# Optimization experiments

Hardware: AMD Instinct MI355X
Metric: run time of the kernel (lower is better)

## Reference

```python
import jax, jax.numpy as jnp
import numpy as np
from jax import lax

EPS = 1e-20

def _conv(x, w, b):
    # stride-2 conv, padding=1, NCHW/OIHW (torch Conv2d semantics)
    y = lax.conv_general_dilated(x, w, (2, 2), ((1, 1), (1, 1)),
                                 dimension_numbers=('NCHW', 'OIHW', 'NCHW'))
    return y + b[None, :, None, None]

def _deconv(x, w, b):
    # ConvTranspose2d(k=4, s=2, p=1): doubles spatial dims (== SAME transpose padding)
    y = lax.conv_transpose(x, w, (2, 2), 'SAME',
                           dimension_numbers=('NCHW', 'OIHW', 'NCHW'))
    return y + b[None, :, None, None]

def _enc_switch(h, win, bin_, wout, bout, wsw, bsw, gnoise):
    r = jax.nn.relu(h)
    hid = jnp.einsum('bd,kds->bks', r, win) + bin_            # [B,K,S]
    y_logits = jnp.einsum('bks,ks->bk', hid, wsw) + bsw       # [B,K]
    g = -jnp.log(gnoise + EPS)                                # Gumbel noise
    y_soft = jax.nn.softmax(y_logits + g, axis=1)
    y_index = jnp.argmax(y_soft, axis=1)                      # [B]
    one_hot = jax.nn.one_hot(y_index, y_logits.shape[1], dtype=y_soft.dtype)
    y_hard = one_hot - lax.stop_gradient(y_soft) + y_soft     # straight-through
    outs = jnp.einsum('bks,ksd->bkd', hid, wout) + bout       # [B,K,192]
    out = jnp.take_along_axis(outs, y_index[:, None, None], axis=1)[:, 0]
    gate = jnp.take_along_axis(y_hard, y_index[:, None], axis=1)  # [B,1] (training gate)
    return h + out * gate, y_logits, y_index, y_hard

def _dec_switch(h, win, bin_, wout, bout, y_index, y_hard):
    r = jax.nn.relu(h)
    hid = jnp.einsum('bd,kds->bks', r, win) + bin_
    outs = jnp.einsum('bks,ksd->bkd', hid, wout) + bout
    out = jnp.take_along_axis(outs, y_index[:, None, None], axis=1)[:, 0]
    gate = jnp.take_along_axis(y_hard, y_index[:, None], axis=1)
    return h + out * gate

def setup_inputs() -> dict:
    key = jax.random.key(0)
    B, C, L, D, K, S = 1024, 3, 10, 192, 10, 10
    ks = jax.random.split(key, 48)
    def n(i, shape, s=0.05):
        return jax.random.normal(ks[i], shape, jnp.float32) * s
    return {
        'x': jax.random.uniform(ks[0], (B, C, 64, 64), jnp.float32),
        'gnoise': jax.random.exponential(ks[1], (L, B, K)).astype(jnp.float32),
        'znoise': jax.random.normal(ks[2], (B, L), jnp.float32),
        'cw1': n(3, (32, C, 4, 4)), 'cb1': n(4, (32,)),
        'cw2': n(5, (32, 32, 4, 4)), 'cb2': n(6, (32,)),
        'cw3': n(7, (64, 32, 4, 4)), 'cb3': n(8, (64,)),
        'cw4': n(9, (64, 64, 4, 4)), 'cb4': n(10, (64,)),
        'fc_w': n(11, (1024, D)), 'fc_b': n(12, (D,)),
        'ein_w': n(13, (L, K, D, S)), 'ein_b': n(14, (L, K, S)),
        'eout_w': n(15, (L, K, S, D)), 'eout_b': n(16, (L, K, D)),
        'esw_w': n(17, (L, K, S)), 'esw_b': n(18, (L, K)),
        'mean_w': n(19, (D, L)), 'mean_b': n(20, (L,)),
        'lv_w': n(21, (D, L)), 'lv_b': n(22, (L,)),
        'fcl_w': n(23, (L, D)), 'fcl_b': n(24, (D,)),
        'din_w': n(25, (L, K, D, S)), 'din_b': n(26, (L, K, S)),
        'dout_w': n(27, (L, K, S, D)), 'dout_b': n(28, (L, K, D)),
        'dfc_w': n(29, (D, 1024)), 'dfc_b': n(30, (1024,)),
        'dw1': n(31, (64, 64, 4, 4)), 'db1': n(32, (64,)),
        'dw2': n(33, (32, 64, 4, 4)), 'db2': n(34, (32,)),
        'dw3': n(35, (32, 32, 4, 4)), 'db3': n(36, (32,)),
        'dw4': n(37, (C, 32, 4, 4)), 'db4': n(38, (C,)),
    }

def reference(x, gnoise, znoise, cw1, cb1, cw2, cb2, cw3, cb3, cw4, cb4,
              fc_w, fc_b, ein_w, ein_b, eout_w, eout_b, esw_w, esw_b,
              mean_w, mean_b, lv_w, lv_b, fcl_w, fcl_b,
              din_w, din_b, dout_w, dout_b, dfc_w, dfc_b,
              dw1, db1, dw2, db2, dw3, db3, dw4, db4):
    # ---- encoder convs ----
    h = jax.nn.relu(_conv(x, cw1, cb1))
    h = jax.nn.relu(_conv(h, cw2, cb2))
    h = jax.nn.relu(_conv(h, cw3, cb3))
    h = jax.nn.relu(_conv(h, cw4, cb4))           # [B,64,4,4]
    h = h.reshape(-1, 1024) @ fc_w + fc_b         # [B,192]
    # ---- encoder FC switches (sequential over latents) ----
    L = ein_w.shape[0]
    ys_index, ys_hard = [], []
    for i in range(L):
        h, _, yi, yh = _enc_switch(h, ein_w[i], ein_b[i], eout_w[i], eout_b[i],
                                   esw_w[i], esw_b[i], gnoise[i])
        ys_index.append(yi); ys_hard.append(yh)
    r = jax.nn.relu(h)
    z_mean = r @ mean_w + mean_b
    z_logvar = r @ lv_w + lv_b
    # ---- reparameterize ----
    z = znoise * jnp.exp(z_logvar / 2) + z_mean
    # ---- decoder ----
    d = z @ fcl_w + fcl_b
    for i in range(L):
        d = _dec_switch(d, din_w[i], din_b[i], dout_w[i], dout_b[i],
                        ys_index[i], ys_hard[i])
    d = jax.nn.relu(d)
    d = jax.nn.relu(d @ dfc_w + dfc_b)
    d = d.reshape(-1, 64, 4, 4)
    d = jax.nn.relu(_deconv(d, dw1, db1))
    d = jax.nn.relu(_deconv(d, dw2, db2))
    d = jax.nn.relu(_deconv(d, dw3, db3))
    recon_x = _deconv(d, dw4, db4)                # [B,C,64,64] logits
    return recon_x, z, z_mean, z_logvar
```

## Files before the change

kernel.cpp:

```cpp
#include <hip/hip_runtime.h>
#include <hip/hip_bf16.h>
#include <math.h>


#define BATCH 1024

using short8 = __attribute__((ext_vector_type(8))) short;
using f32x4  = __attribute__((ext_vector_type(4))) float;

__device__ __forceinline__ ushort f2bf(float f) {
    uint u = __float_as_uint(f);
    uint r = (u + 0x7fffu + ((u >> 16) & 1u)) >> 16;
    return (ushort)r;
}
__device__ __forceinline__ float bf2f(ushort u) {
    return __uint_as_float(((uint)u) << 16);
}
constexpr int ilog2(int v) { return v <= 1 ? 0 : 1 + ilog2(v >> 1); }

__device__ __forceinline__ void conv_frag_elem(const float* __restrict__ w,
                                               ushort* __restrict__ frag,
                                               int idx, int CIN, int COUT) {
    int NCH = CIN / 32, NT = COUT / 16;
    int j = idx & 7; int lane = (idx >> 3) & 63; int rest = idx >> 9;
    int ntile = rest % NT; rest /= NT;
    int ch = rest % NCH; int tap = rest / NCH;
    int o = ntile * 16 + (lane & 15);
    int i = ch * 32 + (lane >> 4) * 8 + j;
    frag[idx] = f2bf(w[((size_t)(o * CIN + i)) * 16 + tap]);
}
__device__ __forceinline__ void deconv_frag_elem(const float* __restrict__ w,
                                                 ushort* __restrict__ frag,
                                                 int idx, int CIN, int COUT) {
    int NCH = CIN / 32, NT = COUT / 16;
    int j = idx & 7; int lane = (idx >> 3) & 63; int rest = idx >> 9;
    int ntile = rest % NT; rest /= NT;
    int ch = rest % NCH; rest /= NCH;
    int tapidx = rest % 4; int cls = rest / 4;
    int py = cls >> 1, px = cls & 1, a = tapidx >> 1, b = tapidx & 1;
    int tap = (py + 2 * a) * 4 + (px + 2 * b);
    int o = ntile * 16 + (lane & 15);
    int i = ch * 32 + (lane >> 4) * 8 + j;
    frag[idx] = f2bf(w[((size_t)(o * CIN + i)) * 16 + tap]);
}

__global__ __launch_bounds__(256)
void prep_all(const float* __restrict__ cw1, const float* __restrict__ cw2,
              const float* __restrict__ cw3, const float* __restrict__ cw4,
              const float* __restrict__ dw1, const float* __restrict__ dw2,
              const float* __restrict__ dw3, const float* __restrict__ dw4,
              const float* __restrict__ ein_w, const float* __restrict__ fc_w,
              const float* __restrict__ dfc_w,
              ushort* __restrict__ c1g, ushort* __restrict__ c2g,
              ushort* __restrict__ c3g, ushort* __restrict__ c4g,
              ushort* __restrict__ d1g, ushort* __restrict__ d2g,
              ushort* __restrict__ d3g, ushort* __restrict__ d4g,
              ushort* __restrict__ encwTb, ushort* __restrict__ fc1g,
              ushort* __restrict__ dfcg) {
    const int b = blockIdx.x, t = threadIdx.x;
    if (b < 8) {
        int idx = b * 256 + t;
        if (idx < 2048) {
            int j = idx & 7; int lane = (idx >> 3) & 63;
            int ntile = (idx >> 9) & 1; int s = idx >> 10;
            int o = ntile * 16 + (lane & 15);
            int kg = lane >> 4;
            int tap = s * 8 + kg * 2 + (j >> 2);
            int c = j & 3;
            c1g[idx] = (c < 3) ? f2bf(cw1[((size_t)(o * 3 + c)) * 16 + tap]) : (ushort)0;
        }
    } else if (b < 72) {
        conv_frag_elem(cw2, c2g, (b - 8) * 256 + t, 32, 32);
    } else if (b < 200) {
        conv_frag_elem(cw3, c3g, (b - 72) * 256 + t, 32, 64);
    } else if (b < 456) {
        conv_frag_elem(cw4, c4g, (b - 200) * 256 + t, 64, 64);
    } else if (b < 712) {
        deconv_frag_elem(dw1, d1g, (b - 456) * 256 + t, 64, 64);
    } else if (b < 840) {
        deconv_frag_elem(dw2, d2g, (b - 712) * 256 + t, 64, 32);
    } else if (b < 904) {
        deconv_frag_elem(dw3, d3g, (b - 840) * 256 + t, 32, 32);
    } else if (b < 936) {
        int idx = (b - 904) * 256 + t;
        if (idx < 8192) {
            int j = idx & 7; int lane = (idx >> 3) & 63; int rest = idx >> 9;
            int tapidx = rest & 3; int cls = rest >> 2;
            int py = cls >> 1, px = cls & 1, a = tapidx >> 1, bb = tapidx & 1;
            int tap = (py + 2 * a) * 4 + (px + 2 * bb);
            int o = lane & 15;
            int i = (lane >> 4) * 8 + j;
            d4g[idx] = (o < 3) ? f2bf(dw4[((size_t)(o * 32 + i)) * 16 + tap]) : (ushort)0;
        }
    } else if (b < 1686) {
        int idx = (b - 936) * 256 + t;
        if (idx < 192000) {
            int ks = idx % 100;
            int d = (idx / 100) % 192;
            int l = idx / 19200;
            int k = ks / 10, s = ks % 10;
            encwTb[idx] = f2bf(ein_w[(size_t)l * 19200 + k * 1920 + d * 10 + s]);
        }
    } else if (b < 2454) {
        int idx = (b - 1686) * 256 + t;
        int jj = idx & 7; int lane = (idx >> 3) & 63; int rest = idx >> 9;
        int nt = rest % 12, s = rest / 12;
        int k_nat = s * 32 + (lane >> 4) * 8 + jj;
        int d = (k_nat & 63) * 16 + (k_nat >> 6);
        int j = nt * 16 + (lane & 15);
        fc1g[idx] = f2bf(fc_w[(size_t)d * 192 + j]);
    } else {
        int idx = (b - 2454) * 256 + t;
        int jj = idx & 7; int lane = (idx >> 3) & 63; int rest = idx >> 9;
        int nt = rest % 64, s = rest / 64;
        int k = s * 32 + (lane >> 4) * 8 + jj;
        int j_nat = nt * 16 + (lane & 15);
        int d = (j_nat & 63) * 16 + (j_nat >> 6);
        dfcg[idx] = f2bf(dfc_w[(size_t)k * 1024 + d]);
    }
}

__global__ __launch_bounds__(256)
void conv12_fused(const float* __restrict__ x, const ushort* __restrict__ w1frag,
                  const float* __restrict__ b1, const ushort* __restrict__ w2frag,
                  const float* __restrict__ b2, ushort* __restrict__ out) {
    __shared__ ushort mid[576 * 40];
    const int t = threadIdx.x;
    const int lane = t & 63, w = t >> 6;
    const int m = lane & 15, kg = lane >> 4;
    const int h = blockIdx.x & 1, n = blockIdx.x >> 1;
    const int base = 16 * h - 1;
    const float* xb = x + (size_t)n * 12288;

    short8 bf1[4];
    #pragma unroll
    for (int f = 0; f < 4; ++f)
        bf1[f] = *(const short8*)(w1frag + (f << 9) + lane * 8);

    for (int mt = w; mt < 36; mt += 4) {
        const int lp = mt * 16 + m;
        const int lx = lp & 31, lyy = lp >> 5;
        const int my = base + lyy;
        const int iy0 = 2 * my - 1, ix0 = 2 * lx - 1;
        short8 av[2];
        #pragma unroll
        for (int s = 0; s < 2; ++s) {
            short8 a;
            #pragma unroll
            for (int tt = 0; tt < 2; ++tt) {
                const int tap = s * 8 + kg * 2 + tt;
                const int ky = tap >> 2, kx = tap & 3;
                const int iy = iy0 + ky, ix = ix0 + kx;
                float v0 = 0.f, v1 = 0.f, v2 = 0.f;
                if ((unsigned)iy < 64u && (unsigned)ix < 64u) {
                    const float* xr = xb + ((iy << 6) + ix);
                    v0 = xr[0]; v1 = xr[4096]; v2 = xr[8192];
                }
                a[4 * tt + 0] = (short)f2bf(v0);
                a[4 * tt + 1] = (short)f2bf(v1);
                a[4 * tt + 2] = (short)f2bf(v2);
                a[4 * tt + 3] = 0;
            }
            av[s] = a;
        }
        f32x4 acc[2] = {{0,0,0,0},{0,0,0,0}};
        #pragma unroll
        for (int s = 0; s < 2; ++s)
            #pragma unroll
            for (int nt = 0; nt < 2; ++nt)
                acc[nt] = __builtin_amdgcn_mfma_f32_16x16x32_bf16(av[s], bf1[s * 2 + nt], acc[nt], 0, 0, 0);
        #pragma unroll
        for (int nt = 0; nt < 2; ++nt) {
            const int och = (nt << 4) + m;
            const float bv = b1[och];
            #pragma unroll
            for (int r = 0; r < 4; ++r) {
                const int lpr = (mt << 4) + (kg << 2) + r;
                mid[(size_t)lpr * 40 + och] = f2bf(fmaxf(acc[nt][r] + bv, 0.f));
            }
        }
    }
    __syncthreads();
    for (int it = 0; it < 4; ++it) {
        const int u = it * 4 + w;
        const int nt = u & 1, mt2 = u >> 1;
        const int p2 = (mt2 << 4) + m;
        const int ox2 = p2 & 15, ly2 = p2 >> 4;
        const int oy2 = 8 * h + ly2;
        const int iy0 = 2 * oy2 - 1, ix0 = 2 * ox2 - 1;
        f32x4 acc = {0, 0, 0, 0};
        const ushort* wl = w2frag + ((size_t)nt << 9) + lane * 8;
        #pragma unroll
        for (int ky = 0; ky < 4; ++ky) {
            const int iy = iy0 + ky;
            const bool vy = (unsigned)iy < 32u;
            const int liy = iy - base;
            #pragma unroll
            for (int kx = 0; kx < 4; ++kx) {
                const int ix = ix0 + kx;
                const bool v = vy && ((unsigned)ix < 32u);
                short8 a = {0, 0, 0, 0, 0, 0, 0, 0};
                if (v) a = *(const short8*)(mid + (size_t)((liy << 5) + ix) * 40 + kg * 8);
                const short8 b = *(const short8*)(wl + ((size_t)((ky * 4 + kx) * 2) << 9));
                acc = __builtin_amdgcn_mfma_f32_16x16x32_bf16(a, b, acc, 0, 0, 0);
            }
        }
        const int och = (nt << 4) + m;
        const float bv = b2[och];
        ushort* ob = out + ((size_t)n * 256 + 128 * h + (mt2 << 4) + (kg << 2)) * 32;
        #pragma unroll
        for (int r = 0; r < 4; ++r)
            ob[r * 32 + och] = f2bf(fmaxf(acc[r] + bv, 0.f));
    }
}

template<int CIN, int COUT, int HIN, int WIN, int NTW, bool RELU>
__global__ __launch_bounds__(256)
void conv_mfma(const ushort* __restrict__ in, const ushort* __restrict__ wfrag,
               const float* __restrict__ bias, ushort* __restrict__ out) {
    constexpr int HOUT = HIN / 2, WOUT = WIN / 2, NCH = CIN / 32, NT = COUT / 16;
    constexpr int NTG = NT / NTW;
    constexpr int LW = ilog2(WOUT), LH = ilog2(HOUT);
    const int lane = threadIdx.x & 63;
    const int gw = (blockIdx.x << 2) + (threadIdx.x >> 6);
    const int ntg = gw % NTG;
    const int mtile = gw / NTG;
    const int m = lane & 15, kg = lane >> 4;
    const int p = (mtile << 4) + m;
    const int ox = p & (WOUT - 1), oy = (p >> LW) & (HOUT - 1), n = p >> (LW + LH);
    const ushort* ibase = in + (size_t)n * (HIN * WIN * CIN);
    const int iy0 = 2 * oy - 1, ix0 = 2 * ox - 1;
    f32x4 acc[NTW];
    #pragma unroll
    for (int nt = 0; nt < NTW; ++nt) acc[nt] = (f32x4){0, 0, 0, 0};
    const ushort* wl = wfrag + ((size_t)(ntg * NTW) << 9) + lane * 8;
    #pragma unroll
    for (int ky = 0; ky < 4; ++ky) {
        const int iy = iy0 + ky;
        const bool vy = (unsigned)iy < (unsigned)HIN;
        #pragma unroll
        for (int kx = 0; kx < 4; ++kx) {
            const int ix = ix0 + kx;
            const bool v = vy && ((unsigned)ix < (unsigned)WIN);
            const int tap = ky * 4 + kx;
            #pragma unroll
            for (int ch = 0; ch < NCH; ++ch) {
                short8 a = {0, 0, 0, 0, 0, 0, 0, 0};
                if (v) a = *(const short8*)(ibase + (size_t)(iy * WIN + ix) * CIN + ch * 32 + kg * 8);
                #pragma unroll
                for (int nt = 0; nt < NTW; ++nt) {
                    const short8 b = *(const short8*)(wl + ((size_t)((tap * NCH + ch) * NT + nt) << 9));
                    acc[nt] = __builtin_amdgcn_mfma_f32_16x16x32_bf16(a, b, acc[nt], 0, 0, 0);
                }
            }
        }
    }
    ushort* ob = out + (size_t)((mtile << 4) + (kg << 2)) * COUT;
    #pragma unroll
    for (int nt = 0; nt < NTW; ++nt) {
        const int och = ((ntg * NTW + nt) << 4) + m;
        const float bv = bias[och];
        #pragma unroll
        for (int r = 0; r < 4; ++r) {
            float vv = acc[nt][r] + bv;
            if (RELU) vv = fmaxf(vv, 0.f);
            ob[r * COUT + och] = f2bf(vv);
        }
    }
}

template<int CIN, int COUT, int HIN, int WIN, int NTW, bool RELU>
__global__ __launch_bounds__(256)
void deconv_mfma_fused(const ushort* __restrict__ in, const ushort* __restrict__ wfrag,
                       const float* __restrict__ bias, ushort* __restrict__ out) {
    constexpr int HOUT = 2 * HIN, WOUT = 2 * WIN, NCH = CIN / 32, NT = COUT / 16;
    constexpr int NTG = NT / NTW;
    constexpr int LW = ilog2(WIN), LH = ilog2(HIN);
    const int lane = threadIdx.x & 63;
    const int gw = (blockIdx.x << 2) + (threadIdx.x >> 6);
    const int ntg = gw % NTG;
    const int mtile = gw / NTG;
    const int m = lane & 15, kg = lane >> 4;
    const int q = (mtile << 4) + m;
    const int oxh = q & (WIN - 1), oyh = (q >> LW) & (HIN - 1), n = q >> (LW + LH);
    const ushort* ibase = in + (size_t)n * (HIN * WIN * CIN);
    f32x4 acc[4][NTW];
    #pragma unroll
    for (int c = 0; c < 4; ++c)
        #pragma unroll
        for (int nt = 0; nt < NTW; ++nt) acc[c][nt] = (f32x4){0, 0, 0, 0};
    const ushort* wl = wfrag + ((size_t)(ntg * NTW) << 9) + lane * 8;
    #pragma unroll
    for (int ch = 0; ch < NCH; ++ch) {
        short8 nb[3][3];
        #pragma unroll
        for (int dy = 0; dy < 3; ++dy) {
            const int iy = oyh + dy - 1;
            const bool vy = (unsigned)iy < (unsigned)HIN;
            #pragma unroll
            for (int dx = 0; dx < 3; ++dx) {
                const int ix = oxh + dx - 1;
                short8 a = {0, 0, 0, 0, 0, 0, 0, 0};
                if (vy && (unsigned)ix < (unsigned)WIN)
                    a = *(const short8*)(ibase + (size_t)(iy * WIN + ix) * CIN + ch * 32 + kg * 8);
                nb[dy][dx] = a;
            }
        }
        #pragma unroll
        for (int cls = 0; cls < 4; ++cls) {
            const int py = cls >> 1, px = cls & 1;
            #pragma unroll
            for (int ti = 0; ti < 4; ++ti) {
                const int a2 = ti >> 1, b2 = ti & 1;
                #pragma unroll
                for (int nt = 0; nt < NTW; ++nt) {
                    const short8 b = *(const short8*)(wl + ((size_t)(((cls * 4 + ti) * NCH + ch) * NT + nt) << 9));
                    acc[cls][nt] = __builtin_amdgcn_mfma_f32_16x16x32_bf16(nb[py + a2][px + b2], b, acc[cls][nt], 0, 0, 0);
                }
            }
        }
    }
    #pragma unroll
    for (int nt = 0; nt < NTW; ++nt) {
        const int och = ((ntg * NTW + nt) << 4) + m;
        const float bv = bias[och];
        #pragma unroll
        for (int cls = 0; cls < 4; ++cls) {
            const int py = cls >> 1, px = cls & 1;
            #pragma unroll
            for (int r = 0; r < 4; ++r) {
                const int qq = (mtile << 4) + (kg << 2) + r;
                const int oxh2 = qq & (WIN - 1), oyh2 = (qq >> LW) & (HIN - 1), n2 = qq >> (LW + LH);
                const int oy = 2 * oyh2 + py, ox = 2 * oxh2 + px;
                float vv = acc[cls][nt][r] + bv;
                if (RELU) vv = fmaxf(vv, 0.f);
                out[(size_t)((n2 * HOUT + oy) * WOUT + ox) * COUT + och] = f2bf(vv);
            }
        }
    }
}

__global__ __launch_bounds__(256)
void deconv34_fused(const ushort* __restrict__ in, const ushort* __restrict__ w3frag,
                    const float* __restrict__ b3, const ushort* __restrict__ w4frag,
                    const float* __restrict__ b4, float* __restrict__ out) {
    __shared__ ushort mid[20 * 32 * 32];
    const int t = threadIdx.x;
    const int lane = t & 63, w = t >> 6;
    const int m = lane & 15, kg = lane >> 4;
    const int h = blockIdx.x & 1, n = blockIdx.x >> 1;
    const int base = 16 * h - 2;
    const ushort* ibase = in + ((size_t)n << 13);

    for (int u = w; u < 20; u += 4) {
        const int nt = u & 1, mt = u >> 1;
        const int ir = 8 * h - 1 + mt;
        short8 nb[3][3];
        #pragma unroll
        for (int dy = 0; dy < 3; ++dy) {
            const int iy = ir + dy - 1;
            const bool vy = (unsigned)iy < 16u;
            #pragma unroll
            for (int dx = 0; dx < 3; ++dx) {
                const int ix = m + dx - 1;
                short8 a = {0, 0, 0, 0, 0, 0, 0, 0};
                if (vy && (unsigned)ix < 16u)
                    a = *(const short8*)(ibase + (size_t)((iy << 4) + ix) * 32 + kg * 8);
                nb[dy][dx] = a;
            }
        }
        const ushort* wl = w3frag + ((size_t)nt << 9) + lane * 8;
        f32x4 acc[4] = {{0,0,0,0},{0,0,0,0},{0,0,0,0},{0,0,0,0}};
        #pragma unroll
        for (int cls = 0; cls < 4; ++cls) {
            const int py = cls >> 1, px = cls & 1;
            #pragma unroll
            for (int ti = 0; ti < 4; ++ti) {
                const int a2 = ti >> 1, b2 = ti & 1;
                const short8 b = *(const short8*)(wl + ((size_t)((cls * 4 + ti) * 2) << 9));
                acc[cls] = __builtin_amdgcn_mfma_f32_16x16x32_bf16(nb[py + a2][px + b2], b, acc[cls], 0, 0, 0);
            }
        }
        const int och = (nt << 4) + m;
        const float bv = b3[och];
        #pragma unroll
        for (int cls = 0; cls < 4; ++cls) {
            const int py = cls >> 1, px = cls & 1;
            const int ly = 2 * mt + py;
            #pragma unroll
            for (int r = 0; r < 4; ++r) {
                const int ox = ((kg << 3) + 2 * r) + px;
                mid[(size_t)((ly << 5) + ox) * 32 + och] = f2bf(fmaxf(acc[cls][r] + bv, 0.f));
            }
        }
    }
    __syncthreads();
    for (int it = 0; it < 8; ++it) {
        const int mt2 = it * 4 + w;
        const int oyh = 16 * h + (mt2 >> 1);
        const int oxh = ((mt2 & 1) << 4) + m;
        short8 nb[3][3];
        #pragma unroll
        for (int dy = 0; dy < 3; ++dy) {
            const int iy = oyh + dy - 1;
            const bool vy = (unsigned)iy < 32u;
            const int ly = iy - base;
            #pragma unroll
            for (int dx = 0; dx < 3; ++dx) {
                const int ix = oxh + dx - 1;
                short8 a = {0, 0, 0, 0, 0, 0, 0, 0};
                if (vy && (unsigned)ix < 32u)
                    a = *(const short8*)(mid + (size_t)((ly << 5) + ix) * 32 + kg * 8);
                nb[dy][dx] = a;
            }
        }
        f32x4 acc[4] = {{0,0,0,0},{0,0,0,0},{0,0,0,0},{0,0,0,0}};
        const ushort* wl = w4frag + lane * 8;
        #pragma unroll
        for (int cls = 0; cls < 4; ++cls) {
            const int py = cls >> 1, px = cls & 1;
            #pragma unroll
            for (int ti = 0; ti < 4; ++ti) {
                const int a2 = ti >> 1, b2 = ti & 1;
                const short8 b = *(const short8*)(wl + ((cls * 4 + ti) << 9));
                acc[cls] = __builtin_amdgcn_mfma_f32_16x16x32_bf16(nb[py + a2][px + b2], b, acc[cls], 0, 0, 0);
            }
        }
        if (m < 3) {
            const float bv = b4[m];
            float* ob = out + (size_t)n * 12288 + m * 4096;
            #pragma unroll
            for (int r = 0; r < 4; ++r) {
                const int x = ((mt2 & 1) << 4) + (kg << 2) + r;
                #pragma unroll
                for (int py = 0; py < 2; ++py) {
                    float2 v = {acc[py * 2 + 0][r] + bv, acc[py * 2 + 1][r] + bv};
                    *(float2*)(ob + (2 * oyh + py) * 64 + 2 * x) = v;
                }
            }
        }
    }
}

__global__ __launch_bounds__(256)
void fc1_mfma(const ushort* __restrict__ in, const ushort* __restrict__ frag,
              const float* __restrict__ bias, float* __restrict__ out) {
    const int lane = threadIdx.x & 63;
    const int gw = (blockIdx.x << 2) + (threadIdx.x >> 6);
    const int nt = gw % 12, mt = gw / 12;
    const int m = lane & 15, kg = lane >> 4;
    const ushort* arow = in + ((size_t)(mt * 16 + m) << 10) + kg * 8;
    const ushort* wl = frag + nt * 512 + lane * 8;
    f32x4 acc0 = {0, 0, 0, 0}, acc1 = {0, 0, 0, 0};
    #pragma unroll
    for (int s = 0; s < 32; s += 2) {
        const short8 a0 = *(const short8*)(arow + s * 32);
        const short8 a1 = *(const short8*)(arow + s * 32 + 32);
        const short8 b0 = *(const short8*)(wl + ((size_t)(s * 12) << 9));
        const short8 b1 = *(const short8*)(wl + ((size_t)((s + 1) * 12) << 9));
        acc0 = __builtin_amdgcn_mfma_f32_16x16x32_bf16(a0, b0, acc0, 0, 0, 0);
        acc1 = __builtin_amdgcn_mfma_f32_16x16x32_bf16(a1, b1, acc1, 0, 0, 0);
    }
    const int j = nt * 16 + m;
    const float bv = bias[j];
    #pragma unroll
    for (int r = 0; r < 4; ++r)
        out[(size_t)(mt * 16 + kg * 4 + r) * 192 + j] = (acc0[r] + acc1[r]) + bv;
}

__global__ __launch_bounds__(256)
void dfc_mfma(const ushort* __restrict__ in, const ushort* __restrict__ frag,
              const float* __restrict__ bias, ushort* __restrict__ out) {
    const int lane = threadIdx.x & 63;
    const int gw = (blockIdx.x << 2) + (threadIdx.x >> 6);
    const int ntg = gw & 15, mt = gw >> 4;
    const int m = lane & 15, kg = lane >> 4;
    const ushort* arow = in + (size_t)(mt * 16 + m) * 192 + kg * 8;
    const ushort* wl = frag + ((size_t)(ntg * 4) << 9) + lane * 8;
    f32x4 acc[4] = {{0,0,0,0},{0,0,0,0},{0,0,0,0},{0,0,0,0}};
    #pragma unroll
    for (int s = 0; s < 6; ++s) {
        const short8 a = *(const short8*)(arow + s * 32);
        #pragma unroll
        for (int q = 0; q < 4; ++q) {
            const short8 b = *(const short8*)(wl + ((size_t)(s * 64 + q) << 9));
            acc[q] = __builtin_amdgcn_mfma_f32_16x16x32_bf16(a, b, acc[q], 0, 0, 0);
        }
    }
    #pragma unroll
    for (int q = 0; q < 4; ++q) {
        const int j_nat = (ntg * 4 + q) * 16 + m;
        const int d = (j_nat & 63) * 16 + (j_nat >> 6);
        const float bv = bias[d];
        #pragma unroll
        for (int r = 0; r < 4; ++r) {
            const float vv = fmaxf(acc[q][r] + bv, 0.f);
            out[((size_t)(mt * 16 + kg * 4 + r) << 10) + j_nat] = f2bf(vv);
        }
    }
}

__global__ __launch_bounds__(256)
void enc_switch4(float* __restrict__ h,
                 const ushort* __restrict__ winTb,
                 const float* __restrict__ bin_all,
                 const float* __restrict__ wout_all,
                 const float* __restrict__ bout_all,
                 const float* __restrict__ wsw_all,
                 const float* __restrict__ bsw_all,
                 const float* __restrict__ gn_all,
                 int* __restrict__ yidx, float* __restrict__ gateArr) {
    const int t = threadIdx.x;
    const int b0 = blockIdx.x << 2;
    __shared__ float hold[4][192], r[4][192], part[4][200], hid[4][100], lg[4][10];
    __shared__ int yi_s[4]; __shared__ float gate_s[4];
    if (t < 192) {
        #pragma unroll
        for (int row = 0; row < 4; ++row) {
            const float v = h[(size_t)(b0 + row) * 192 + t];
            hold[row][t] = v; r[row][t] = fmaxf(v, 0.f);
        }
    }
    for (int i = 0; i < 10; ++i) {
        __syncthreads();
        if (t < 200) {
            const int ks = (t < 100) ? t : t - 100;
            const int half = (t < 100) ? 0 : 1;
            const ushort* wp = winTb + (size_t)i * 19200 + (half * 96) * 100 + ks;
            const float* r0 = &r[0][half * 96];
            const float* r1 = &r[1][half * 96];
            const float* r2 = &r[2][half * 96];
            const float* r3 = &r[3][half * 96];
            float a0 = 0.f, a1 = 0.f, a2 = 0.f, a3 = 0.f;
            #pragma unroll
            for (int dd = 0; dd < 96; ++dd) {
                const float wv = bf2f(wp[dd * 100]);
                a0 = fmaf(r0[dd], wv, a0);
                a1 = fmaf(r1[dd], wv, a1);
                a2 = fmaf(r2[dd], wv, a2);
                a3 = fmaf(r3[dd], wv, a3);
            }
            part[0][t] = a0; part[1][t] = a1; part[2][t] = a2; part[3][t] = a3;
        }
        __syncthreads();
        if (t < 100) {
            const float bv = bin_all[i * 100 + t];
            #pragma unroll
            for (int row = 0; row < 4; ++row)
                hid[row][t] = part[row][t] + part[row][t + 100] + bv;
        }
        __syncthreads();
        if (t < 40) {
            const int row = t / 10, k = t % 10;
            const float* wsw = wsw_all + i * 100 + k * 10;
            float acc = bsw_all[i * 10 + k];
            #pragma unroll
            for (int s = 0; s < 10; ++s) acc = fmaf(hid[row][k * 10 + s], wsw[s], acc);
            lg[row][k] = acc - logf(gn_all[(size_t)i * 10240 + (b0 + row) * 10 + k] + 1e-20f);
        }
        __syncthreads();
        if (t < 4) {
            int bi = 0; float best = lg[t][0];
            #pragma unroll
            for (int k = 1; k < 10; ++k) if (lg[t][k] > best) { best = lg[t][k]; bi = k; }
            float sum = 0.f;
            #pragma unroll
            for (int k = 0; k < 10; ++k) sum += expf(lg[t][k] - best);
            const float ysoft = 1.0f / sum;
            yi_s[t] = bi;
            const float g = (1.0f - ysoft) + ysoft;
            gate_s[t] = g;
            yidx[i * 1024 + b0 + t] = bi;
            gateArr[i * 1024 + b0 + t] = g;
        }
        __syncthreads();
        if (t < 192) {
            #pragma unroll
            for (int row = 0; row < 4; ++row) {
                const int yi = yi_s[row];
                const float gate = gate_s[row];
                const float* wb = wout_all + (size_t)i * 19200 + yi * 1920 + t;
                float acc = bout_all[i * 1920 + yi * 192 + t];
                #pragma unroll
                for (int s = 0; s < 10; ++s) acc = fmaf(hid[row][yi * 10 + s], wb[s * 192], acc);
                const float nv = hold[row][t] + acc * gate;
                hold[row][t] = nv; r[row][t] = fmaxf(nv, 0.f);
            }
        }
    }
    __syncthreads();
    if (t < 192) {
        #pragma unroll
        for (int row = 0; row < 4; ++row)
            h[(size_t)(b0 + row) * 192 + t] = hold[row][t];
    }
}

__global__ __launch_bounds__(256)
void dec_switch_all(const float* __restrict__ h,
                    const float* __restrict__ win_all,
                    const float* __restrict__ bin_all,
                    const float* __restrict__ wout_all,
                    const float* __restrict__ bout_all,
                    const int* __restrict__ yidx, const float* __restrict__ gateArr,
                    ushort* __restrict__ dbf) {
    const int b = blockIdx.x, t = threadIdx.x;
    __shared__ float hold[192], r[192], part[240], hid[10];
    if (t < 192) { float v = h[(size_t)b * 192 + t]; hold[t] = v; r[t] = fmaxf(v, 0.f); }
    for (int i = 0; i < 10; ++i) {
        const int yi = yidx[i * 1024 + b];
        const float gate = gateArr[i * 1024 + b];
        __syncthreads();
        if (t < 240) {
            const int s = t % 10, g = t / 10;
            const float* wp = win_all + (size_t)i * 19200 + yi * 1920 + s;
            const int d0 = g * 8;
            float a0 = 0.f, a1 = 0.f;
            #pragma unroll
            for (int dd = 0; dd < 8; dd += 2) {
                a0 = fmaf(r[d0 + dd + 0], wp[(d0 + dd + 0) * 10], a0);
                a1 = fmaf(r[d0 + dd + 1], wp[(d0 + dd + 1) * 10], a1);
            }
            part[t] = a0 + a1;
        }
        __syncthreads();
        if (t < 10) {
            float acc = bin_all[i * 100 + yi * 10 + t];
            #pragma unroll
            for (int g = 0; g < 24; ++g) acc += part[g * 10 + t];
            hid[t] = acc;
        }
        __syncthreads();
        if (t < 192) {
            const float* wp = wout_all + (size_t)i * 19200 + yi * 1920 + t;
            float acc = bout_all[i * 1920 + yi * 192 + t];
            #pragma unroll
            for (int s = 0; s < 10; ++s) acc = fmaf(hid[s], wp[s * 192], acc);
            float nv = hold[t] + acc * gate;
            hold[t] = nv; r[t] = fmaxf(nv, 0.f);
        }
    }
    if (t < 192) dbf[(size_t)b * 192 + t] = f2bf(r[t]);
}

__global__ __launch_bounds__(192)
void zfcl_kernel(const float* __restrict__ h,
                 const float* __restrict__ mw, const float* __restrict__ mb,
                 const float* __restrict__ lw, const float* __restrict__ lb,
                 const float* __restrict__ zn,
                 const float* __restrict__ fw, const float* __restrict__ fb,
                 float* __restrict__ out_z, float* __restrict__ out_mean,
                 float* __restrict__ out_lv, float* __restrict__ dbuf) {
    const int b = blockIdx.x, t = threadIdx.x;
    __shared__ float r[192], pm[160], pl[160], zsh[10];
    for (int d = t; d < 192; d += 192) r[d] = fmaxf(h[(size_t)b * 192 + d], 0.f);
    __syncthreads();
    if (t < 160) {
        const int l = t % 10, g = t / 10;
        float am = 0.f, al = 0.f;
        #pragma unroll
        for (int d = g * 12; d < g * 12 + 12; ++d) {
            am = fmaf(r[d], mw[d * 10 + l], am);
            al = fmaf(r[d], lw[d * 10 + l], al);
        }
        pm[t] = am; pl[t] = al;
    }
    __syncthreads();
    if (t < 10) {
        float zm = mb[t], zl = lb[t];
        #pragma unroll
        for (int g = 0; g < 16; ++g) { zm += pm[g * 10 + t]; zl += pl[g * 10 + t]; }
        const float z = zn[(size_t)b * 10 + t] * expf(zl * 0.5f) + zm;
        out_mean[(size_t)b * 10 + t] = zm;
        out_lv[(size_t)b * 10 + t] = zl;
        out_z[(size_t)b * 10 + t] = z;
        zsh[t] = z;
    }
    __syncthreads();
    for (int d = t; d < 192; d += 192) {
        float acc = fb[d];
        #pragma unroll
        for (int l = 0; l < 10; ++l) acc = fmaf(zsh[l], fw[l * 192 + d], acc);
        dbuf[(size_t)b * 192 + d] = acc;
    }
}

extern "C" void kernel_launch(void* const* d_in, const int* in_sizes, int n_in,
                              void* d_out, int out_size, void* d_ws, size_t ws_size,
                              hipStream_t stream) {
    const float* x      = (const float*)d_in[0];
    const float* gnoise = (const float*)d_in[1];
    const float* znoise = (const float*)d_in[2];
    const float* cw1 = (const float*)d_in[3];  const float* cb1 = (const float*)d_in[4];
    const float* cw2 = (const float*)d_in[5];  const float* cb2 = (const float*)d_in[6];
    const float* cw3 = (const float*)d_in[7];  const float* cb3 = (const float*)d_in[8];
    const float* cw4 = (const float*)d_in[9];  const float* cb4 = (const float*)d_in[10];
    const float* fc_w = (const float*)d_in[11]; const float* fc_b = (const float*)d_in[12];
    const float* ein_w = (const float*)d_in[13]; const float* ein_b = (const float*)d_in[14];
    const float* eout_w = (const float*)d_in[15]; const float* eout_b = (const float*)d_in[16];
    const float* esw_w = (const float*)d_in[17]; const float* esw_b = (const float*)d_in[18];
    const float* mean_w = (const float*)d_in[19]; const float* mean_b = (const float*)d_in[20];
    const float* lv_w = (const float*)d_in[21]; const float* lv_b = (const float*)d_in[22];
    const float* fcl_w = (const float*)d_in[23]; const float* fcl_b = (const float*)d_in[24];
    const float* din_w = (const float*)d_in[25]; const float* din_b = (const float*)d_in[26];
    const float* dout_w = (const float*)d_in[27]; const float* dout_b = (const float*)d_in[28];
    const float* dfc_w = (const float*)d_in[29]; const float* dfc_b = (const float*)d_in[30];
    const float* dw1 = (const float*)d_in[31]; const float* db1 = (const float*)d_in[32];
    const float* dw2 = (const float*)d_in[33]; const float* db2 = (const float*)d_in[34];
    const float* dw3 = (const float*)d_in[35]; const float* db3 = (const float*)d_in[36];
    const float* dw4 = (const float*)d_in[37]; const float* db4 = (const float*)d_in[38];

    float* out = (float*)d_out;
    float* recon  = out;
    float* z_out  = out + 12582912;
    float* zm_out = z_out + 10240;
    float* zl_out = zm_out + 10240;

    char* ws = (char*)d_ws;
    ushort* bufB  = (ushort*)(ws + 100663296);
    ushort* bufC  = (ushort*)(ws + 117440512);
    ushort* bufD  = (ushort*)(ws + 125829120);
    float*  bufH  = (float*) (ws + 127926272);
    float*  bufD2 = (float*) (ws + 128712704);
    int*    yidx  = (int*)   (ws + 129499136);
    float*  gate  = (float*) (ws + 129540096);
    char*   fb    = ws + 129581056;
    ushort* c1g = (ushort*)(fb);
    ushort* c2g = (ushort*)(fb + 4096);
    ushort* c3g = (ushort*)(fb + 36864);
    ushort* c4g = (ushort*)(fb + 102400);
    ushort* d1g = (ushort*)(fb + 233472);
    ushort* d2g = (ushort*)(fb + 364544);
    ushort* d3g = (ushort*)(fb + 430080);
    ushort* d4g = (ushort*)(fb + 462848);
    ushort* encwTb = (ushort*)(fb + 479232);
    ushort* fc1g  = (ushort*)(fb + 1247232);
    ushort* dfcg  = (ushort*)(fb + 1640448);
    ushort* dbf   = (ushort*)(fb + 2033664);

    prep_all<<<3222, 256, 0, stream>>>(cw1, cw2, cw3, cw4, dw1, dw2, dw3, dw4,
                                       ein_w, fc_w, dfc_w,
                                       c1g, c2g, c3g, c4g, d1g, d2g, d3g, d4g,
                                       encwTb, fc1g, dfcg);

    conv12_fused<<<2048, 256, 0, stream>>>(x, c1g, cb1, c2g, cb2, bufB);
    conv_mfma<32, 64, 16, 16, 4, true><<<1024, 256, 0, stream>>>(bufB, c3g, cb3, bufC);
    conv_mfma<64, 64, 8, 8, 4, true><<<256, 256, 0, stream>>>(bufC, c4g, cb4, bufD);
    fc1_mfma<<<192, 256, 0, stream>>>(bufD, fc1g, fc_b, bufH);
    enc_switch4<<<256, 256, 0, stream>>>(bufH, encwTb, ein_b, eout_w, eout_b,
                                         esw_w, esw_b, gnoise, yidx, gate);
    zfcl_kernel<<<1024, 192, 0, stream>>>(bufH, mean_w, mean_b, lv_w, lv_b,
                                          znoise, fcl_w, fcl_b,
                                          z_out, zm_out, zl_out, bufD2);
    dec_switch_all<<<1024, 256, 0, stream>>>(bufD2, din_w, din_b, dout_w, dout_b,
                                             yidx, gate, dbf);
    dfc_mfma<<<256, 256, 0, stream>>>(dbf, dfcg, dfc_b, bufD);

    deconv_mfma_fused<64, 64, 4, 4, 4, true><<<256, 256, 0, stream>>>(bufD, d1g, db1, bufC);
    deconv_mfma_fused<64, 32, 8, 8, 2, true><<<1024, 256, 0, stream>>>(bufC, d2g, db2, bufB);
    deconv34_fused<<<2048, 256, 0, stream>>>(bufB, d3g, db3, d4g, db4, recon);
}
```

Baseline: 264.5 us.

## Fuse conv3+conv4 and deconv1+deconv2 into per-sample kernels with LDS intermediates

Replaces the separate conv3/conv4 and deconv1/deconv2 launches with two fused kernels. Each block handles one sample and keeps the intermediate activation in shared memory instead of writing it to global memory. This removes two launches and a global round trip for the intermediates. The cost is that each block runs two stages serially with a barrier between them, and parallelism per layer changes: conv4 and deconv1 now use 4 waves per sample.

```diff
diff --git a/kernel.cpp b/kernel.cpp
--- a/kernel.cpp
+++ b/kernel.cpp
@@ -16,7 +16,6 @@
 __device__ __forceinline__ float bf2f(ushort u) {
     return __uint_as_float(((uint)u) << 16);
 }
-constexpr int ilog2(int v) { return v <= 1 ? 0 : 1 + ilog2(v >> 1); }
 
 __device__ __forceinline__ void conv_frag_elem(const float* __restrict__ w,
                                                ushort* __restrict__ frag,
@@ -214,127 +213,184 @@
     }
 }
 
-template<int CIN, int COUT, int HIN, int WIN, int NTW, bool RELU>
 __global__ __launch_bounds__(256)
-void conv_mfma(const ushort* __restrict__ in, const ushort* __restrict__ wfrag,
-               const float* __restrict__ bias, ushort* __restrict__ out) {
-    constexpr int HOUT = HIN / 2, WOUT = WIN / 2, NCH = CIN / 32, NT = COUT / 16;
-    constexpr int NTG = NT / NTW;
-    constexpr int LW = ilog2(WOUT), LH = ilog2(HOUT);
-    const int lane = threadIdx.x & 63;
-    const int gw = (blockIdx.x << 2) + (threadIdx.x >> 6);
-    const int ntg = gw % NTG;
-    const int mtile = gw / NTG;
+void conv34_fused(const ushort* __restrict__ in, const ushort* __restrict__ w3frag,
+                  const float* __restrict__ b3, const ushort* __restrict__ w4frag,
+                  const float* __restrict__ b4, ushort* __restrict__ out) {
+    __shared__ ushort mid[64 * 64];
+    const int t = threadIdx.x;
+    const int lane = t & 63, w = t >> 6;
     const int m = lane & 15, kg = lane >> 4;
-    const int p = (mtile << 4) + m;
-    const int ox = p & (WOUT - 1), oy = (p >> LW) & (HOUT - 1), n = p >> (LW + LH);
-    const ushort* ibase = in + (size_t)n * (HIN * WIN * CIN);
-    const int iy0 = 2 * oy - 1, ix0 = 2 * ox - 1;
-    f32x4 acc[NTW];
-    #pragma unroll
-    for (int nt = 0; nt < NTW; ++nt) acc[nt] = (f32x4){0, 0, 0, 0};
-    const ushort* wl = wfrag + ((size_t)(ntg * NTW) << 9) + lane * 8;
-    #pragma unroll
-    for (int ky = 0; ky < 4; ++ky) {
-        const int iy = iy0 + ky;
-        const bool vy = (unsigned)iy < (unsigned)HIN;
-        #pragma unroll
-        for (int kx = 0; kx < 4; ++kx) {
-            const int ix = ix0 + kx;
-            const bool v = vy && ((unsigned)ix < (unsigned)WIN);
-            const int tap = ky * 4 + kx;
-            #pragma unroll
-            for (int ch = 0; ch < NCH; ++ch) {
+    const int n = blockIdx.x;
+    const ushort* ibase = in + ((size_t)n << 13);
+
+    {
+        const int p = (w << 4) + m;
+        const int ox = p & 7, oy = p >> 3;
+        const int iy0 = 2 * oy - 1, ix0 = 2 * ox - 1;
+        f32x4 acc[4] = {{0,0,0,0},{0,0,0,0},{0,0,0,0},{0,0,0,0}};
+        #pragma unroll
+        for (int ky = 0; ky < 4; ++ky) {
+            const int iy = iy0 + ky;
+            const bool vy = (unsigned)iy < 16u;
+            #pragma unroll
+            for (int kx = 0; kx < 4; ++kx) {
+                const int ix = ix0 + kx;
+                const bool v = vy && ((unsigned)ix < 16u);
                 short8 a = {0, 0, 0, 0, 0, 0, 0, 0};
-                if (v) a = *(const short8*)(ibase + (size_t)(iy * WIN + ix) * CIN + ch * 32 + kg * 8);
+                if (v) a = *(const short8*)(ibase + (size_t)((iy << 4) + ix) * 32 + kg * 8);
+                const int tap = ky * 4 + kx;
                 #pragma unroll
-                for (int nt = 0; nt < NTW; ++nt) {
-                    const short8 b = *(const short8*)(wl + ((size_t)((tap * NCH + ch) * NT + nt) << 9));
+                for (int nt = 0; nt < 4; ++nt) {
+                    const short8 b = *(const short8*)(w3frag + ((size_t)(tap * 4 + nt) << 9) + lane * 8);
                     acc[nt] = __builtin_amdgcn_mfma_f32_16x16x32_bf16(a, b, acc[nt], 0, 0, 0);
                 }
             }
         }
-    }
-    ushort* ob = out + (size_t)((mtile << 4) + (kg << 2)) * COUT;
-    #pragma unroll
-    for (int nt = 0; nt < NTW; ++nt) {
-        const int och = ((ntg * NTW + nt) << 4) + m;
-        const float bv = bias[och];
-        #pragma unroll
-        for (int r = 0; r < 4; ++r) {
-            float vv = acc[nt][r] + bv;
-            if (RELU) vv = fmaxf(vv, 0.f);
-            ob[r * COUT + och] = f2bf(vv);
-        }
-    }
-}
-
-template<int CIN, int COUT, int HIN, int WIN, int NTW, bool RELU>
+        #pragma unroll
+        for (int nt = 0; nt < 4; ++nt) {
+            const int och = (nt << 4) + m;
+            const float bv = b3[och];
+            #pragma unroll
+            for (int r = 0; r < 4; ++r) {
+                const int pr = (w << 4) + (kg << 2) + r;
+                mid[(size_t)pr * 64 + och] = f2bf(fmaxf(acc[nt][r] + bv, 0.f));
+            }
+        }
+    }
+    __syncthreads();
+    {
+        const int ox = m & 3, oy = m >> 2;
+        const int iy0 = 2 * oy - 1, ix0 = 2 * ox - 1;
+        f32x4 acc = {0, 0, 0, 0};
+        const ushort* wl = w4frag + ((size_t)w << 9) + lane * 8;
+        #pragma unroll
+        for (int ky = 0; ky < 4; ++ky) {
+            const int iy = iy0 + ky;
+            const bool vy = (unsigned)iy < 8u;
+            #pragma unroll
+            for (int kx = 0; kx < 4; ++kx) {
+                const int ix = ix0 + kx;
+                const bool v = vy && ((unsigned)ix < 8u);
+                const int tap = ky * 4 + kx;
+                #pragma unroll
+                for (int ch = 0; ch < 2; ++ch) {
+                    short8 a = {0, 0, 0, 0, 0, 0, 0, 0};
+                    if (v) a = *(const short8*)(mid + (size_t)((iy << 3) + ix) * 64 + ch * 32 + kg * 8);
+                    const short8 b = *(const short8*)(wl + ((size_t)((tap * 2 + ch) * 4) << 9));
+                    acc = __builtin_amdgcn_mfma_f32_16x16x32_bf16(a, b, acc, 0, 0, 0);
+                }
+            }
+        }
+        const int och = (w << 4) + m;
+        const float bv = b4[och];
+        #pragma unroll
+        for (int r = 0; r < 4; ++r)
+            out[((size_t)n * 16 + (kg << 2) + r) * 64 + och] = f2bf(fmaxf(acc[r] + bv, 0.f));
+    }
+}
+
 __global__ __launch_bounds__(256)
-void deconv_mfma_fused(const ushort* __restrict__ in, const ushort* __restrict__ wfrag,
-                       const float* __restrict__ bias, ushort* __restrict__ out) {
-    constexpr int HOUT = 2 * HIN, WOUT = 2 * WIN, NCH = CIN / 32, NT = COUT / 16;
-    constexpr int NTG = NT / NTW;
-    constexpr int LW = ilog2(WIN), LH = ilog2(HIN);
-    const int lane = threadIdx.x & 63;
-    const int gw = (blockIdx.x << 2) + (threadIdx.x >> 6);
-    const int ntg = gw % NTG;
-    const int mtile = gw / NTG;
+void deconv12_fused(const ushort* __restrict__ in, const ushort* __restrict__ w1frag,
+                    const float* __restrict__ b1, const ushort* __restrict__ w2frag,
+                    const float* __restrict__ b2, ushort* __restrict__ out) {
+    __shared__ ushort mid[64 * 64];
+    const int t = threadIdx.x;
+    const int lane = t & 63, w = t >> 6;
     const int m = lane & 15, kg = lane >> 4;
-    const int q = (mtile << 4) + m;
-    const int oxh = q & (WIN - 1), oyh = (q >> LW) & (HIN - 1), n = q >> (LW + LH);
-    const ushort* ibase = in + (size_t)n * (HIN * WIN * CIN);
-    f32x4 acc[4][NTW];
-    #pragma unroll
-    for (int c = 0; c < 4; ++c)
-        #pragma unroll
-        for (int nt = 0; nt < NTW; ++nt) acc[c][nt] = (f32x4){0, 0, 0, 0};
-    const ushort* wl = wfrag + ((size_t)(ntg * NTW) << 9) + lane * 8;
-    #pragma unroll
-    for (int ch = 0; ch < NCH; ++ch) {
-        short8 nb[3][3];
-        #pragma unroll
-        for (int dy = 0; dy < 3; ++dy) {
-            const int iy = oyh + dy - 1;
-            const bool vy = (unsigned)iy < (unsigned)HIN;
-            #pragma unroll
-            for (int dx = 0; dx < 3; ++dx) {
-                const int ix = oxh + dx - 1;
-                short8 a = {0, 0, 0, 0, 0, 0, 0, 0};
-                if (vy && (unsigned)ix < (unsigned)WIN)
-                    a = *(const short8*)(ibase + (size_t)(iy * WIN + ix) * CIN + ch * 32 + kg * 8);
-                nb[dy][dx] = a;
-            }
-        }
+    const int n = blockIdx.x;
+    const ushort* ibase = in + ((size_t)n << 10);
+
+    {
+        const int oxh = m & 3, oyh = m >> 2;
+        f32x4 acc[4] = {{0,0,0,0},{0,0,0,0},{0,0,0,0},{0,0,0,0}};
+        const ushort* wl = w1frag + ((size_t)w << 9) + lane * 8;
+        #pragma unroll
+        for (int ch = 0; ch < 2; ++ch) {
+            short8 nb[3][3];
+            #pragma unroll
+            for (int dy = 0; dy < 3; ++dy) {
+                const int iy = oyh + dy - 1;
+                const bool vy = (unsigned)iy < 4u;
+                #pragma unroll
+                for (int dx = 0; dx < 3; ++dx) {
+                    const int ix = oxh + dx - 1;
+                    short8 a = {0, 0, 0, 0, 0, 0, 0, 0};
+                    if (vy && (unsigned)ix < 4u)
+                        a = *(const short8*)(ibase + (size_t)((iy << 2) + ix) * 64 + ch * 32 + kg * 8);
+                    nb[dy][dx] = a;
+                }
+            }
+            #pragma unroll
+            for (int cls = 0; cls < 4; ++cls) {
+                const int py = cls >> 1, px = cls & 1;
+                #pragma unroll
+                for (int ti = 0; ti < 4; ++ti) {
+                    const int a2 = ti >> 1, b2i = ti & 1;
+                    const short8 b = *(const short8*)(wl + ((size_t)(((cls * 4 + ti) * 2 + ch) * 4) << 9));
+                    acc[cls] = __builtin_amdgcn_mfma_f32_16x16x32_bf16(nb[py + a2][px + b2i], b, acc[cls], 0, 0, 0);
+                }
+            }
+        }
+        const int och = (w << 4) + m;
+        const float bv = b1[och];
         #pragma unroll
         for (int cls = 0; cls < 4; ++cls) {
             const int py = cls >> 1, px = cls & 1;
             #pragma unroll
-            for (int ti = 0; ti < 4; ++ti) {
-                const int a2 = ti >> 1, b2 = ti & 1;
+            for (int r = 0; r < 4; ++r) {
+                const int qq = (kg << 2) + r;
+                const int oxh2 = qq & 3, oyh2 = qq >> 2;
+                const int oy = 2 * oyh2 + py, ox = 2 * oxh2 + px;
+                mid[(size_t)((oy << 3) + ox) * 64 + och] = f2bf(fmaxf(acc[cls][r] + bv, 0.f));
+            }
+        }
+    }
+    __syncthreads();
+    for (int u = w; u < 8; u += 4) {
+        const int nt = u & 1, mt = u >> 1;
+        const int q = (mt << 4) + m;
+        const int oxh = q & 7, oyh = q >> 3;
+        f32x4 acc[4] = {{0,0,0,0},{0,0,0,0},{0,0,0,0},{0,0,0,0}};
+        const ushort* wl = w2frag + ((size_t)nt << 9) + lane * 8;
+        #pragma unroll
+        for (int ch = 0; ch < 2; ++ch) {
+            short8 nb[3][3];
+            #pragma unroll
+            for (int dy = 0; dy < 3; ++dy) {
+                const int iy = oyh + dy - 1;
+                const bool vy = (unsigned)iy < 8u;
                 #pragma unroll
-                for (int nt = 0; nt < NTW; ++nt) {
-                    const short8 b = *(const short8*)(wl + ((size_t)(((cls * 4 + ti) * NCH + ch) * NT + nt) << 9));
-                    acc[cls][nt] = __builtin_amdgcn_mfma_f32_16x16x32_bf16(nb[py + a2][px + b2], b, acc[cls][nt], 0, 0, 0);
+                for (int dx = 0; dx < 3; ++dx) {
+                    const int ix = oxh + dx - 1;
+                    short8 a = {0, 0, 0, 0, 0, 0, 0, 0};
+                    if (vy && (unsigned)ix < 8u)
+                        a = *(const short8*)(mid + (size_t)((iy << 3) + ix) * 64 + ch * 32 + kg * 8);
+                    nb[dy][dx] = a;
                 }
             }
-        }
-    }
-    #pragma unroll
-    for (int nt = 0; nt < NTW; ++nt) {
-        const int och = ((ntg * NTW + nt) << 4) + m;
-        const float bv = bias[och];
+            #pragma unroll
+            for (int cls = 0; cls < 4; ++cls) {
+                const int py = cls >> 1, px = cls & 1;
+                #pragma unroll
+                for (int ti = 0; ti < 4; ++ti) {
+                    const int a2 = ti >> 1, b2i = ti & 1;
+                    const short8 b = *(const short8*)(wl + ((size_t)(((cls * 4 + ti) * 2 + ch) * 2) << 9));
+                    acc[cls] = __builtin_amdgcn_mfma_f32_16x16x32_bf16(nb[py + a2][px + b2i], b, acc[cls], 0, 0, 0);
+                }
+            }
+        }
+        const int och = (nt << 4) + m;
+        const float bv = b2[och];
         #pragma unroll
         for (int cls = 0; cls < 4; ++cls) {
             const int py = cls >> 1, px = cls & 1;
             #pragma unroll
             for (int r = 0; r < 4; ++r) {
-                const int qq = (mtile << 4) + (kg << 2) + r;
-                const int oxh2 = qq & (WIN - 1), oyh2 = (qq >> LW) & (HIN - 1), n2 = qq >> (LW + LH);
+                const int qq = (mt << 4) + (kg << 2) + r;
+                const int oxh2 = qq & 7, oyh2 = qq >> 3;
                 const int oy = 2 * oyh2 + py, ox = 2 * oxh2 + px;
-                float vv = acc[cls][nt][r] + bv;
-                if (RELU) vv = fmaxf(vv, 0.f);
-                out[(size_t)((n2 * HOUT + oy) * WOUT + ox) * COUT + och] = f2bf(vv);
+                out[((size_t)(n * 16 + oy) * 16 + ox) * 32 + och] = f2bf(fmaxf(acc[cls][r] + bv, 0.f));
             }
         }
     }
@@ -718,7 +774,6 @@
 
     char* ws = (char*)d_ws;
     ushort* bufB  = (ushort*)(ws + 100663296);
-    ushort* bufC  = (ushort*)(ws + 117440512);
     ushort* bufD  = (ushort*)(ws + 125829120);
     float*  bufH  = (float*) (ws + 127926272);
     float*  bufD2 = (float*) (ws + 128712704);
@@ -744,8 +799,7 @@
                                        encwTb, fc1g, dfcg);
 
     conv12_fused<<<2048, 256, 0, stream>>>(x, c1g, cb1, c2g, cb2, bufB);
-    conv_mfma<32, 64, 16, 16, 4, true><<<1024, 256, 0, stream>>>(bufB, c3g, cb3, bufC);
-    conv_mfma<64, 64, 8, 8, 4, true><<<256, 256, 0, stream>>>(bufC, c4g, cb4, bufD);
+    conv34_fused<<<1024, 256, 0, stream>>>(bufB, c3g, cb3, c4g, cb4, bufD);
     fc1_mfma<<<192, 256, 0, stream>>>(bufD, fc1g, fc_b, bufH);
     enc_switch4<<<256, 256, 0, stream>>>(bufH, encwTb, ein_b, eout_w, eout_b,
                                          esw_w, esw_b, gnoise, yidx, gate);
@@ -756,7 +810,6 @@
                                              yidx, gate, dbf);
     dfc_mfma<<<256, 256, 0, stream>>>(dbf, dfcg, dfc_b, bufD);
 
-    deconv_mfma_fused<64, 64, 4, 4, 4, true><<<256, 256, 0, stream>>>(bufD, d1g, db1, bufC);
-    deconv_mfma_fused<64, 32, 8, 8, 2, true><<<1024, 256, 0, stream>>>(bufC, d2g, db2, bufB);
+    deconv12_fused<<<1024, 256, 0, stream>>>(bufD, d1g, db1, d2g, db2, bufB);
     deconv34_fused<<<2048, 256, 0, stream>>>(bufB, d3g, db3, d4g, db4, recon);
 }
```

Result: faster. 224.8 us (-15.0%).
